# Performance work log

Hardware: AMD Instinct MI355X
Metric: run time of the kernel (lower is better)

Reference implementation:

```python
import jax, jax.numpy as jnp
import numpy as np

B, S, D_IN, D_OUT, H = 1, 4096, 1024, 1024, 16
HD = D_OUT // H


def setup_inputs() -> dict:
    key = jax.random.key(0)
    ks = jax.random.split(key, 6)
    sc = 0.02
    return {
        "x": jax.random.normal(ks[0], (B, S, D_IN), dtype=jnp.float32),
        "Wq": jax.random.normal(ks[1], (D_IN, D_OUT), dtype=jnp.float32) * sc,
        "Wk": jax.random.normal(ks[2], (D_IN, D_OUT), dtype=jnp.float32) * sc,
        "Wv": jax.random.normal(ks[3], (D_IN, D_OUT), dtype=jnp.float32) * sc,
        "Wo": jax.random.normal(ks[4], (D_OUT, D_OUT), dtype=jnp.float32) * sc,
        "bo": jnp.zeros((D_OUT,), dtype=jnp.float32),
    }


def reference(x, Wq, Wk, Wv, Wo, bo):
    b, n, _ = x.shape
    # QKV projections (no bias), split into heads: [b, h, n, hd]
    def heads(w):
        return (x @ w).reshape(b, n, H, HD).transpose(0, 2, 1, 3)
    q, k, v = heads(Wq), heads(Wk), heads(Wv)
    # scores [b, h, n, n], causal mask, scaled softmax (dropout p=0 -> identity)
    scores = jnp.einsum("bhqd,bhkd->bhqk", q, k)
    causal = jnp.tril(jnp.ones((n, n), dtype=bool))
    scores = jnp.where(causal, scores, -jnp.inf)
    attn = jax.nn.softmax(scores / jnp.sqrt(jnp.float32(HD)), axis=-1)
    ctx = jnp.einsum("bhqk,bhkd->bhqd", attn, v)
    ctx = ctx.transpose(0, 2, 1, 3).reshape(b, n, D_OUT)
    return ctx @ Wo + bo
```

## Files before the change

### kernel.cpp

```cpp
#include <hip/hip_runtime.h>
#include <hip/hip_bf16.h>
#include <stdint.h>


typedef __bf16 bf16;
typedef __bf16 bf16x4 __attribute__((ext_vector_type(4)));
typedef __bf16 bf16x8 __attribute__((ext_vector_type(8)));
typedef float  f32x4  __attribute__((ext_vector_type(4)));

#define MFMA32(a, b, c) __builtin_amdgcn_mfma_f32_16x16x32_bf16((a), (b), (c), 0, 0, 0)

static constexpr int S_LEN  = 4096;
static constexpr int DMODEL = 1024;
static constexpr int HDIM   = 64;
static constexpr int LDQK   = 2048;

#define GLOAD_LDS16(g, l)                                                      \
  __builtin_amdgcn_global_load_lds((__attribute__((address_space(1))) void*)(g), \
                                   (__attribute__((address_space(3))) void*)(l), 16, 0, 0)

__global__ __launch_bounds__(256) void preprocess(const float* __restrict__ x,
                                                  const float* __restrict__ Wq,
                                                  const float* __restrict__ Wk,
                                                  const float* __restrict__ Wv,
                                                  const float* __restrict__ Wo,
                                                  bf16* __restrict__ xb,
                                                  bf16* __restrict__ Wt,
                                                  bf16* __restrict__ Wot) {
  __shared__ float tile[64][65];
  const int t = threadIdx.x, b = blockIdx.x;
  if (b < 1024) {
#pragma unroll
    for (int i = 0; i < 4; i++) {
      int idx = b * 1024 + i * 256 + t;
      float4 v = ((const float4*)x)[idx];
      bf16x4 o;
      o[0] = (bf16)v.x; o[1] = (bf16)v.y; o[2] = (bf16)v.z; o[3] = (bf16)v.w;
      ((bf16x4*)xb)[idx] = o;
    }
    return;
  }
  const int id = b - 1024;
  const int wsel = id >> 8;
  const int t2 = id & 255;
  const int kb = (t2 & 15) * 64, nb = (t2 >> 4) * 64;
  const float* src = (wsel == 0) ? Wq : (wsel == 1) ? Wk : (wsel == 2) ? Wv : Wo;
  bf16* dst = (wsel < 3) ? (Wt + (size_t)wsel * 1024 * 1024) : Wot;
#pragma unroll
  for (int i = 0; i < 16; i++) {
    int idx = t + i * 256;
    int r = idx >> 6, c = idx & 63;
    tile[r][c] = src[(size_t)(kb + r) * 1024 + nb + c];
  }
  __syncthreads();
#pragma unroll
  for (int i = 0; i < 16; i++) {
    int idx = t + i * 256;
    int cc = idx >> 6, rr = idx & 63;
    dst[(size_t)(nb + cc) * 1024 + kb + rr] = (bf16)tile[rr][cc];
  }
}

__global__ __launch_bounds__(256) void gemm_qkv(const bf16* __restrict__ A,
                                                const bf16* __restrict__ Bt,
                                                bf16* __restrict__ QK,
                                                bf16* __restrict__ Vt) {
  __shared__ bf16 lsA[128 * 32];
  __shared__ bf16 lsB[128 * 32];
  const int tid = threadIdx.x, w = tid >> 6, lane = tid & 63;
  const int l15 = lane & 15, quad = lane >> 4;
  const int m0 = blockIdx.x * 128, n0 = blockIdx.y * 128;
  const int wm = (w >> 1) * 64, wn = (w & 1) * 64;
  const int rowA = lane >> 2;
  const int colk = (lane & 3) * 8;

  f32x4 acc[4][4] = {};

  for (int k0 = 0; k0 < 1024; k0 += 32) {
    __syncthreads();
#pragma unroll
    for (int i = 0; i < 2; i++) {
      int s = w * 2 + i;
      const bf16* ga = A + (size_t)(m0 + s * 16 + rowA) * 1024 + k0 + colk;
      GLOAD_LDS16(ga, lsA + s * 512);
      const bf16* gb = Bt + (size_t)(n0 + s * 16 + rowA) * 1024 + k0 + colk;
      GLOAD_LDS16(gb, lsB + s * 512);
    }
    __syncthreads();

    bf16x8 af[4], bfr[4];
#pragma unroll
    for (int r = 0; r < 4; r++)
      af[r] = *(const bf16x8*)(lsA + (wm + r * 16 + l15) * 32 + quad * 8);
#pragma unroll
    for (int c = 0; c < 4; c++)
      bfr[c] = *(const bf16x8*)(lsB + (wn + c * 16 + l15) * 32 + quad * 8);
#pragma unroll
    for (int r = 0; r < 4; r++)
#pragma unroll
      for (int c = 0; c < 4; c++)
        acc[r][c] = MFMA32(af[r], bfr[c], acc[r][c]);
  }

  if (n0 < 2048) {
#pragma unroll
    for (int r = 0; r < 4; r++) {
#pragma unroll
      for (int c = 0; c < 4; c++) {
        int col = n0 + wn + c * 16 + l15;
        float scale = (col < 1024) ? 0.18033688f : 1.0f;
#pragma unroll
        for (int e = 0; e < 4; e++) {
          int row = m0 + wm + r * 16 + quad * 4 + e;
          QK[(size_t)row * LDQK + col] = (bf16)(acc[r][c][e] * scale);
        }
      }
    }
  } else {
#pragma unroll
    for (int r = 0; r < 4; r++) {
#pragma unroll
      for (int c = 0; c < 4; c++) {
        int vcol = (n0 - 2048) + wn + c * 16 + l15;
        int row0 = m0 + wm + r * 16 + quad * 4;
        bf16x4 pk;
#pragma unroll
        for (int e = 0; e < 4; e++) pk[e] = (bf16)acc[r][c][e];
        *(bf16x4*)(Vt + (size_t)vcol * S_LEN + row0) = pk;
      }
    }
  }
}

__global__ __launch_bounds__(256, 2) void flash_attn(const bf16* __restrict__ QK,
                                                     const bf16* __restrict__ Vt,
                                                     bf16* __restrict__ Ctx) {
  __shared__ float Obuf[4][64][68];
  __shared__ float Lbuf[4][4][64];
  const int tid = threadIdx.x, w = tid >> 6, lane = tid & 63;
  const int l15 = lane & 15, quad = lane >> 4;
  const int hq = blockIdx.y * HDIM;
  const int qt0 = blockIdx.x;
  const int krow0 = w * 32 + ((l15 >> 2) << 3) + (l15 & 3);

  for (int p = 0; p < 2; p++) {
    const int qb = p ? (63 - qt0) : qt0;
    const int T = (qb >> 1) + 1;

    bf16x8 qf[4][2];
#pragma unroll
    for (int qg = 0; qg < 4; qg++)
#pragma unroll
      for (int kk = 0; kk < 2; kk++)
        qf[qg][kk] = *(const bf16x8*)(QK + (size_t)(qb * 64 + qg * 16 + l15) * LDQK +
                                      hq + kk * 32 + quad * 8);

    f32x4 oacc[4][4] = {};
    float lsum[4] = {0.f, 0.f, 0.f, 0.f};

    bf16x8 kf[2][2];
#pragma unroll
    for (int c = 0; c < 2; c++)
#pragma unroll
      for (int kk = 0; kk < 2; kk++)
        kf[c][kk] = *(const bf16x8*)(QK + (size_t)(krow0 + 4 * c) * LDQK +
                                     DMODEL + hq + kk * 32 + quad * 8);

    for (int j = 0; j < T; j++) {
      bf16x8 vf[4];
#pragma unroll
      for (int dg = 0; dg < 4; dg++)
        vf[dg] = *(const bf16x8*)(Vt + (size_t)(hq + dg * 16 + l15) * S_LEN +
                                  j * 128 + w * 32 + quad * 8);

      f32x4 sacc[2][4] = {};
#pragma unroll
      for (int kk = 0; kk < 2; kk++)
#pragma unroll
        for (int c = 0; c < 2; c++)
#pragma unroll
          for (int qg = 0; qg < 4; qg++)
            sacc[c][qg] = MFMA32(kf[c][kk], qf[qg][kk], sacc[c][qg]);

      if (j + 1 < T) {
#pragma unroll
        for (int c = 0; c < 2; c++)
#pragma unroll
          for (int kk = 0; kk < 2; kk++)
            kf[c][kk] = *(const bf16x8*)(QK + (size_t)((j + 1) * 128 + krow0 + 4 * c) * LDQK +
                                         DMODEL + hq + kk * 32 + quad * 8);
      }

      bf16x8 pfr[4];
      if (j == T - 1) {
        const int kb0 = j * 128 + w * 32 + quad * 8;
#pragma unroll
        for (int qg = 0; qg < 4; qg++) {
          const int qrow = qb * 64 + qg * 16 + l15;
          bf16x8 pb;
#pragma unroll
          for (int c = 0; c < 2; c++)
#pragma unroll
            for (int e = 0; e < 4; e++) {
              float s = sacc[c][qg][e];
              if (kb0 + 4 * c + e > qrow) s = -1e30f;
              float pv = __builtin_amdgcn_exp2f(s);
              lsum[qg] += pv;
              pb[c * 4 + e] = (bf16)pv;
            }
          pfr[qg] = pb;
        }
      } else {
#pragma unroll
        for (int qg = 0; qg < 4; qg++) {
          bf16x8 pb;
#pragma unroll
          for (int c = 0; c < 2; c++)
#pragma unroll
            for (int e = 0; e < 4; e++) {
              float pv = __builtin_amdgcn_exp2f(sacc[c][qg][e]);
              lsum[qg] += pv;
              pb[c * 4 + e] = (bf16)pv;
            }
          pfr[qg] = pb;
        }
      }

#pragma unroll
      for (int qg = 0; qg < 4; qg++)
#pragma unroll
        for (int dg = 0; dg < 4; dg++)
          oacc[qg][dg] = MFMA32(pfr[qg], vf[dg], oacc[qg][dg]);
    }

#pragma unroll
    for (int qg = 0; qg < 4; qg++)
#pragma unroll
      for (int dg = 0; dg < 4; dg++)
#pragma unroll
        for (int e = 0; e < 4; e++)
          Obuf[w][qg * 16 + quad * 4 + e][dg * 16 + l15] = oacc[qg][dg][e];
#pragma unroll
    for (int qg = 0; qg < 4; qg++)
      Lbuf[w][quad][qg * 16 + l15] = lsum[qg];
    __syncthreads();

    const int qr = w * 16 + (lane >> 2);
    const int dsg = (lane & 3) * 16;
    f32x4 os[4] = {};
#pragma unroll
    for (int ww = 0; ww < 4; ww++)
#pragma unroll
      for (int i = 0; i < 4; i++)
        os[i] += *(const f32x4*)&Obuf[ww][qr][dsg + i * 4];
    float lr = 0.f;
#pragma unroll
    for (int ww = 0; ww < 4; ww++)
#pragma unroll
      for (int qq = 0; qq < 4; qq++)
        lr += Lbuf[ww][qq][qr];
    const float linv = 1.f / lr;

    bf16x8 o0, o1;
#pragma unroll
    for (int i = 0; i < 8; i++) {
      o0[i] = (bf16)(os[i >> 2][i & 3] * linv);
      o1[i] = (bf16)(os[2 + (i >> 2)][i & 3] * linv);
    }
    bf16* dst = Ctx + (size_t)(qb * 64 + qr) * DMODEL + hq + dsg;
    *(bf16x8*)dst = o0;
    *(bf16x8*)(dst + 8) = o1;
    __syncthreads();
  }
}

__global__ __launch_bounds__(256) void gemm_out(const bf16* __restrict__ A,
                                                const bf16* __restrict__ Bt,
                                                float* __restrict__ C,
                                                const float* __restrict__ bias) {
  __shared__ bf16 lsA[64 * 32];
  __shared__ bf16 lsB[128 * 32];
  const int tid = threadIdx.x, w = tid >> 6, lane = tid & 63;
  const int l15 = lane & 15, quad = lane >> 4;
  const int m0 = blockIdx.x * 64, n0 = blockIdx.y * 128;
  const int wm = (w >> 1) * 32, wn = (w & 1) * 64;
  const int rowA = lane >> 2;
  const int colk = (lane & 3) * 8;

  f32x4 acc[2][4] = {};

  for (int k0 = 0; k0 < 1024; k0 += 32) {
    __syncthreads();
#pragma unroll
    for (int i = 0; i < 3; i++) {
      int s = w * 3 + i;
      if (s < 4) {
        const bf16* ga = A + (size_t)(m0 + s * 16 + rowA) * 1024 + k0 + colk;
        GLOAD_LDS16(ga, lsA + s * 512);
      } else {
        const bf16* gb = Bt + (size_t)(n0 + (s - 4) * 16 + rowA) * 1024 + k0 + colk;
        GLOAD_LDS16(gb, lsB + (s - 4) * 512);
      }
    }
    __syncthreads();

    bf16x8 af[2], bfr[4];
#pragma unroll
    for (int r = 0; r < 2; r++)
      af[r] = *(const bf16x8*)(lsA + (wm + r * 16 + l15) * 32 + quad * 8);
#pragma unroll
    for (int c = 0; c < 4; c++)
      bfr[c] = *(const bf16x8*)(lsB + (wn + c * 16 + l15) * 32 + quad * 8);
#pragma unroll
    for (int r = 0; r < 2; r++)
#pragma unroll
      for (int c = 0; c < 4; c++)
        acc[r][c] = MFMA32(af[r], bfr[c], acc[r][c]);
  }

#pragma unroll
  for (int r = 0; r < 2; r++) {
#pragma unroll
    for (int c = 0; c < 4; c++) {
      int col = n0 + wn + c * 16 + l15;
#pragma unroll
      for (int e = 0; e < 4; e++) {
        int row = m0 + wm + r * 16 + quad * 4 + e;
        C[(size_t)row * 1024 + col] = acc[r][c][e] + bias[col];
      }
    }
  }
}

extern "C" void kernel_launch(void* const* d_in, const int* in_sizes, int n_in,
                              void* d_out, int out_size, void* d_ws, size_t ws_size,
                              hipStream_t stream) {
  const float* x  = (const float*)d_in[0];
  const float* Wq = (const float*)d_in[1];
  const float* Wk = (const float*)d_in[2];
  const float* Wv = (const float*)d_in[3];
  const float* Wo = (const float*)d_in[4];
  const float* bo = (const float*)d_in[5];

  char* ws = (char*)d_ws;
  bf16* xb  = (bf16*)(ws);
  bf16* Wt  = (bf16*)(ws + (8u  << 20));
  bf16* Wot = (bf16*)(ws + (14u << 20));
  bf16* QK  = (bf16*)(ws + (16u << 20));
  bf16* Vt  = (bf16*)(ws + (32u << 20));
  bf16* Ctx = (bf16*)(ws + (40u << 20));

  preprocess<<<2048, 256, 0, stream>>>(x, Wq, Wk, Wv, Wo, xb, Wt, Wot);
  gemm_qkv<<<dim3(32, 24), 256, 0, stream>>>(xb, Wt, QK, Vt);
  flash_attn<<<dim3(32, 16), 256, 0, stream>>>(QK, Vt, Ctx);
  gemm_out<<<dim3(64, 8), 256, 0, stream>>>(Ctx, Wot, (float*)d_out, bo);
}
```

Baseline: 219.9 us.

## Double-buffer K/V fragment loads and shrink flash-attn output reduction LDS

The attention main loop now ping-pongs two register sets of K and V fragments, issuing the loads for the next tile before computing the current one, so global latency is hidden behind the MFMA work. The cross-wave output reduction is split into four 16-row passes through a much smaller LDS buffer. This cuts LDS use per block, which can allow more resident blocks. In exchange the kernel holds more live registers and adds barriers inside the epilogue.

```diff
diff --git a/kernel.cpp b/kernel.cpp
--- a/kernel.cpp
+++ b/kernel.cpp
@@ -135,7 +135,7 @@
 __global__ __launch_bounds__(256, 2) void flash_attn(const bf16* __restrict__ QK,
                                                      const bf16* __restrict__ Vt,
                                                      bf16* __restrict__ Ctx) {
-  __shared__ float Obuf[4][64][68];
+  __shared__ float Obuf[4][16][68];
   __shared__ float Lbuf[4][4][64];
   const int tid = threadIdx.x, w = tid >> 6, lane = tid & 63;
   const int l15 = lane & 15, quad = lane >> 4;
@@ -158,21 +158,21 @@
     f32x4 oacc[4][4] = {};
     float lsum[4] = {0.f, 0.f, 0.f, 0.f};
 
-    bf16x8 kf[2][2];
-#pragma unroll
-    for (int c = 0; c < 2; c++)
-#pragma unroll
-      for (int kk = 0; kk < 2; kk++)
-        kf[c][kk] = *(const bf16x8*)(QK + (size_t)(krow0 + 4 * c) * LDQK +
-                                     DMODEL + hq + kk * 32 + quad * 8);
-
-    for (int j = 0; j < T; j++) {
-      bf16x8 vf[4];
+    auto load_k = [&](int j, bf16x8 (&kf)[2][2]) {
+#pragma unroll
+      for (int c = 0; c < 2; c++)
+#pragma unroll
+        for (int kk = 0; kk < 2; kk++)
+          kf[c][kk] = *(const bf16x8*)(QK + (size_t)(j * 128 + krow0 + 4 * c) * LDQK +
+                                       DMODEL + hq + kk * 32 + quad * 8);
+    };
+    auto load_v = [&](int j, bf16x8 (&vf)[4]) {
 #pragma unroll
       for (int dg = 0; dg < 4; dg++)
         vf[dg] = *(const bf16x8*)(Vt + (size_t)(hq + dg * 16 + l15) * S_LEN +
                                   j * 128 + w * 32 + quad * 8);
-
+    };
+    auto compute = [&](int j, bf16x8 (&kf)[2][2], bf16x8 (&vf)[4]) {
       f32x4 sacc[2][4] = {};
 #pragma unroll
       for (int kk = 0; kk < 2; kk++)
@@ -181,15 +181,6 @@
 #pragma unroll
           for (int qg = 0; qg < 4; qg++)
             sacc[c][qg] = MFMA32(kf[c][kk], qf[qg][kk], sacc[c][qg]);
-
-      if (j + 1 < T) {
-#pragma unroll
-        for (int c = 0; c < 2; c++)
-#pragma unroll
-          for (int kk = 0; kk < 2; kk++)
-            kf[c][kk] = *(const bf16x8*)(QK + (size_t)((j + 1) * 128 + krow0 + 4 * c) * LDQK +
-                                         DMODEL + hq + kk * 32 + quad * 8);
-      }
 
       bf16x8 pfr[4];
       if (j == T - 1) {
@@ -231,46 +222,48 @@
 #pragma unroll
         for (int dg = 0; dg < 4; dg++)
           oacc[qg][dg] = MFMA32(pfr[qg], vf[dg], oacc[qg][dg]);
-    }
-
-#pragma unroll
-    for (int qg = 0; qg < 4; qg++)
-#pragma unroll
-      for (int dg = 0; dg < 4; dg++)
-#pragma unroll
-        for (int e = 0; e < 4; e++)
-          Obuf[w][qg * 16 + quad * 4 + e][dg * 16 + l15] = oacc[qg][dg][e];
+    };
+
+    bf16x8 kfA[2][2], vfA[4], kfB[2][2], vfB[4];
+    load_k(0, kfA); load_v(0, vfA);
+    for (int j = 0; j < T; j += 2) {
+      if (j + 1 < T) { load_k(j + 1, kfB); load_v(j + 1, vfB); }
+      compute(j, kfA, vfA);
+      if (j + 2 < T) { load_k(j + 2, kfA); load_v(j + 2, vfA); }
+      if (j + 1 < T) compute(j + 1, kfB, vfB);
+    }
+
+    __syncthreads();
 #pragma unroll
     for (int qg = 0; qg < 4; qg++)
       Lbuf[w][quad][qg * 16 + l15] = lsum[qg];
-    __syncthreads();
-
-    const int qr = w * 16 + (lane >> 2);
-    const int dsg = (lane & 3) * 16;
-    f32x4 os[4] = {};
-#pragma unroll
-    for (int ww = 0; ww < 4; ww++)
-#pragma unroll
-      for (int i = 0; i < 4; i++)
-        os[i] += *(const f32x4*)&Obuf[ww][qr][dsg + i * 4];
-    float lr = 0.f;
-#pragma unroll
-    for (int ww = 0; ww < 4; ww++)
-#pragma unroll
-      for (int qq = 0; qq < 4; qq++)
-        lr += Lbuf[ww][qq][qr];
-    const float linv = 1.f / lr;
-
-    bf16x8 o0, o1;
-#pragma unroll
-    for (int i = 0; i < 8; i++) {
-      o0[i] = (bf16)(os[i >> 2][i & 3] * linv);
-      o1[i] = (bf16)(os[2 + (i >> 2)][i & 3] * linv);
-    }
-    bf16* dst = Ctx + (size_t)(qb * 64 + qr) * DMODEL + hq + dsg;
-    *(bf16x8*)dst = o0;
-    *(bf16x8*)(dst + 8) = o1;
-    __syncthreads();
+
+    const int row = tid >> 4;
+    const int col = (tid & 15) * 4;
+    for (int qg = 0; qg < 4; qg++) {
+#pragma unroll
+      for (int dg = 0; dg < 4; dg++)
+#pragma unroll
+        for (int e = 0; e < 4; e++)
+          Obuf[w][quad * 4 + e][dg * 16 + l15] = oacc[qg][dg][e];
+      __syncthreads();
+      f32x4 os = {};
+#pragma unroll
+      for (int ww = 0; ww < 4; ww++)
+        os += *(const f32x4*)&Obuf[ww][row][col];
+      float lr = 0.f;
+#pragma unroll
+      for (int ww = 0; ww < 4; ww++)
+#pragma unroll
+        for (int qq = 0; qq < 4; qq++)
+          lr += Lbuf[ww][qq][qg * 16 + row];
+      const float linv = 1.f / lr;
+      bf16x4 ob;
+#pragma unroll
+      for (int e2 = 0; e2 < 4; e2++) ob[e2] = (bf16)(os[e2] * linv);
+      *(bf16x4*)(Ctx + (size_t)(qb * 64 + qg * 16 + row) * DMODEL + hq + col) = ob;
+      __syncthreads();
+    }
   }
 }
 
```

After: 219.1 us. Within noise of the previous version (-0.3%).
